# Kernel tuning notes

Hardware: AMD Instinct MI355X
Metric: run time of the kernel (lower is better)

Reference implementation:

```python
import jax, jax.numpy as jnp
import numpy as np

N_PARTICLES = 3_000_000
N_CVS = 30_000
N_MODELS = 8
FEATS = [64, 64, 64, 64]
E0, E1 = 2.0, 3.0
LN_EPS = 1e-5


def _dihedral(p):
    # p: [4,3] -> scalar dihedral angle (standard atan2 formulation)
    b1 = p[1] - p[0]
    b2 = p[2] - p[1]
    b3 = p[3] - p[2]
    n1 = jnp.cross(b1, b2)
    n2 = jnp.cross(b2, b3)
    m1 = jnp.cross(n1, b2 / jnp.linalg.norm(b2))
    return jnp.arctan2(jnp.dot(m1, n2), jnp.dot(n1, n2))


def _ensemble_energy(cvs, gamma, beta, Ws, bs):
    # cvs: [n_cvs] -> energy per model: [n_models]
    x = jnp.concatenate([jnp.cos(cvs), jnp.sin(cvs)])  # [2*n_cvs]
    mu = jnp.mean(x)
    var = jnp.mean((x - mu) ** 2)
    x = (x - mu) / jnp.sqrt(var + LN_EPS) * gamma + beta  # LayerNorm
    h = x[None, None, :]  # [1,1,2n] broadcasts against [M,2n,f]
    for i in range(len(Ws) - 1):
        h = jax.nn.relu(jnp.matmul(h, Ws[i]) + bs[i])  # [M,1,f]
    h = jnp.matmul(h, Ws[-1]) + bs[-1]  # [M,1,1]
    return h[:, 0, 0]  # [M]  (squeeze(-1) then batch dim 1)


def _uncertainty_weight(model_div):
    iswitch = (E1 - model_div) / (E1 - E0)
    fl = jnp.floor(iswitch)
    smooth = 0.5 * (1.0 + jnp.cos(jnp.pi * (1.0 - iswitch)))
    # heaviside(floor(iswitch), smooth): 1 if floor>0, smooth if floor==0, 0 if floor<0
    return jnp.where(fl > 0, 1.0, jnp.where(fl < 0, 0.0, smooth)).astype(model_div.dtype)


def setup_inputs() -> dict:
    key = jax.random.key(0)
    ks = jax.random.split(key, 16)
    positions = jax.random.normal(ks[0], (N_PARTICLES, 3), jnp.float32) * 3.0
    boxvectors = jnp.diag(jnp.full((3,), 10.0, dtype=jnp.float32))
    colvar_idx = jax.random.randint(ks[1], (N_CVS, 4), 0, N_PARTICLES)
    dims = [2 * N_CVS] + FEATS + [1]
    inp = {"positions": positions, "boxvectors": boxvectors, "colvar_idx": colvar_idx,
           "gamma": jnp.ones((2 * N_CVS,), jnp.float32),
           "beta": jnp.zeros((2 * N_CVS,), jnp.float32)}
    for i in range(5):
        bound = 1.0 / np.sqrt(dims[i])  # kaiming_uniform-like bound
        inp[f"W{i}"] = jax.random.uniform(ks[2 + i], (N_MODELS, dims[i], dims[i + 1]),
                                           jnp.float32, -bound, bound)
        inp[f"b{i}"] = jnp.zeros((N_MODELS, 1, dims[i + 1]), jnp.float32)
    return inp


def reference(positions, boxvectors, colvar_idx, gamma, beta,
              W0, b0, W1, b1, W2, b2, W3, b3, W4, b4):
    Ws = [W0, W1, W2, W3, W4]
    bs = [b0, b1, b2, b3, b4]
    boxsize = jnp.diag(boxvectors)  # [3]
    pos = positions - jnp.floor(positions / boxsize) * boxsize  # PBC wrap
    quads = pos[colvar_idx.reshape(-1)].reshape(-1, 4, 3)  # [n_cvs,4,3]
    cvs, dcvs_dx = jax.vmap(jax.value_and_grad(_dihedral))(quads)  # [n],[n,4,3]

    efn = lambda c: _ensemble_energy(c, gamma, beta, Ws, bs)  # [M]
    energy = efn(cvs)  # [M]
    mean_forces = -jax.jacrev(efn)(cvs)  # [M, n_cvs]: grad of -energy[m] wrt cvs

    model_div = jnp.sqrt(jnp.mean(jnp.var(mean_forces, axis=0, ddof=1)))
    sigma = _uncertainty_weight(model_div)
    mf = jnp.mean(mean_forces, axis=0)  # [n_cvs]
    contrib = (mf[:, None, None] * dcvs_dx).reshape(-1, 3)  # [n_cvs*4,3]
    forces = jnp.zeros_like(pos).at[colvar_idx.reshape(-1)].add(contrib)
    return energy.mean() * sigma, forces * sigma
```

## Files before the change

kernel.cpp:

```cpp
#include <hip/hip_runtime.h>
#include <math.h>

#define NCV   30000
#define NX    60000
#define NM    8
#define LN_EPSF 1e-5f
#define NFORCE 9000000

#define NB_CV 512
#define JB    96
#define SLAB  625
#define NBX   235
#define NB_MF 118

#define WS_XRAW   0
#define WS_DCV    60000
#define WS_G      420000
#define WS_LNP    900000
#define WS_Z0P    901024
#define WS_DZ0    950176
#define WS_E      950688
#define WS_SGP    950696
#define WS_SGXP   952576
#define WS_VARSUM 954456
#define WS_TICKET 954457
#define WS_SIGMA  954458
#define WS_FLAG   954459

struct F3 { float x, y, z; };
__device__ __forceinline__ F3 f3sub(F3 a, F3 b){ return {a.x-b.x, a.y-b.y, a.z-b.z}; }
__device__ __forceinline__ F3 f3add(F3 a, F3 b){ return {a.x+b.x, a.y+b.y, a.z+b.z}; }
__device__ __forceinline__ F3 f3scale(F3 a, float s){ return {a.x*s, a.y*s, a.z*s}; }
__device__ __forceinline__ float f3dot(F3 a, F3 b){ return a.x*b.x + a.y*b.y + a.z*b.z; }
__device__ __forceinline__ F3 f3cross(F3 a, F3 b){
  return { a.y*b.z - a.z*b.y, a.z*b.x - a.x*b.z, a.x*b.y - a.y*b.x };
}

__device__ __forceinline__ void compute_mu_inv(const float* __restrict__ ws, float* out2, int tid) {
  if (tid < 64) {
    float a = 0.f, b = 0.f;
    #pragma unroll 4
    for (int k = tid; k < NB_CV; k += 64) { a += ws[WS_LNP + k]; b += ws[WS_LNP + NB_CV + k]; }
    #pragma unroll
    for (int o = 1; o < 64; o <<= 1) { a += __shfl_xor(a, o); b += __shfl_xor(b, o); }
    if (tid == 0) {
      float mu  = a * (1.f / NX);
      float var = b * (1.f / NX) - mu * mu;
      out2[0] = mu;
      out2[1] = 1.f / sqrtf(var + LN_EPSF);
    }
  }
}

__global__ void k_cv(const float* __restrict__ pos, const float* __restrict__ box,
                     const int* __restrict__ idx, float* __restrict__ ws,
                     float* __restrict__ out) {
  int tid = threadIdx.x;
  int gtid = blockIdx.x * 256 + tid;

  {
    float4 z4 = {0.f, 0.f, 0.f, 0.f};
    float4* fz = (float4*)(out + 4);
    const int NF4 = (NFORCE - 4) / 4;
    for (int i = gtid; i < NF4; i += NB_CV * 256) fz[i] = z4;
    if (gtid == 0) {
      out[1] = 0.f; out[2] = 0.f; out[3] = 0.f; out[NFORCE] = 0.f;
      ws[WS_VARSUM] = 0.f;
      ((unsigned int*)ws)[WS_TICKET] = 0u;
      ((unsigned int*)ws)[WS_FLAG]   = 0u;
    }
  }

  float cx = 0.f, cx2 = 0.f;
  int i = gtid;
  if (i < NCV) {
    float bx = box[0], by = box[4], bz = box[8];
    int4 q4 = *(const int4*)(idx + i*4);
    int pidx[4] = {q4.x, q4.y, q4.z, q4.w};
    F3 p[4];
    #pragma unroll
    for (int a = 0; a < 4; a++) {
      int pi = pidx[a];
      float X = pos[(size_t)pi*3 + 0];
      float Y = pos[(size_t)pi*3 + 1];
      float Z = pos[(size_t)pi*3 + 2];
      X -= floorf(X / bx) * bx;
      Y -= floorf(Y / by) * by;
      Z -= floorf(Z / bz) * bz;
      p[a] = {X, Y, Z};
    }
    F3 b1 = f3sub(p[1], p[0]);
    F3 b2 = f3sub(p[2], p[1]);
    F3 b3 = f3sub(p[3], p[2]);
    F3 n1 = f3cross(b1, b2);
    F3 n2 = f3cross(b2, b3);
    float L = sqrtf(f3dot(b2, b2));
    F3 u = f3scale(b2, 1.f / L);
    F3 m1 = f3cross(n1, u);
    float yv = f3dot(m1, n2);
    float xv = f3dot(n1, n2);
    float h = sqrtf(xv*xv + yv*yv);
    float cphi = xv / h;
    float sphi = yv / h;

    float invd = 1.f / (h*h);
    float dX = -yv * invd;
    float dY =  xv * invd;
    F3 dn1 = f3scale(n2, dX);
    F3 dn2 = f3scale(n1, dX);
    F3 dm1 = f3scale(n2, dY);
    dn2 = f3add(dn2, f3scale(m1, dY));
    dn1 = f3add(dn1, f3cross(u, dm1));
    F3 du = f3cross(dm1, n1);
    float ud = f3dot(u, du);
    F3 db2 = f3scale(f3sub(du, f3scale(u, ud)), 1.f / L);
    db2 = f3add(db2, f3cross(b3, dn2));
    F3 db3 = f3cross(dn2, b2);
    F3 db1 = f3cross(b2, dn1);
    db2 = f3add(db2, f3cross(dn1, b1));

    F3 g0 = f3scale(db1, -1.f);
    F3 g1 = f3sub(db1, db2);
    F3 g2 = f3sub(db2, db3);
    F3 g3 = db3;

    ws[WS_XRAW + i]       = cphi;
    ws[WS_XRAW + NCV + i] = sphi;
    ws[WS_DCV + 0*NCV  + i] = g0.x; ws[WS_DCV + 1*NCV  + i] = g0.y; ws[WS_DCV + 2*NCV  + i] = g0.z;
    ws[WS_DCV + 3*NCV  + i] = g1.x; ws[WS_DCV + 4*NCV  + i] = g1.y; ws[WS_DCV + 5*NCV  + i] = g1.z;
    ws[WS_DCV + 6*NCV  + i] = g2.x; ws[WS_DCV + 7*NCV  + i] = g2.y; ws[WS_DCV + 8*NCV  + i] = g2.z;
    ws[WS_DCV + 9*NCV  + i] = g3.x; ws[WS_DCV + 10*NCV + i] = g3.y; ws[WS_DCV + 11*NCV + i] = g3.z;

    cx  = cphi + sphi;
    cx2 = cphi*cphi + sphi*sphi;
  }

  #pragma unroll
  for (int o = 1; o < 64; o <<= 1) { cx += __shfl_xor(cx, o); cx2 += __shfl_xor(cx2, o); }
  __shared__ float sa[4], sb[4];
  int w = tid >> 6, l = tid & 63;
  if (l == 0) { sa[w] = cx; sb[w] = cx2; }
  __syncthreads();
  if (tid == 0) {
    ws[WS_LNP + blockIdx.x]         = sa[0] + sa[1] + sa[2] + sa[3];
    ws[WS_LNP + NB_CV + blockIdx.x] = sb[0] + sb[1] + sb[2] + sb[3];
  }
}

__global__ __launch_bounds__(256, 2)
void k_z0(const float4* __restrict__ W0, const float* __restrict__ gamma,
          const float* __restrict__ beta, float* __restrict__ ws) {
  __shared__ float stats[2];
  __shared__ float yl[SLAB];
  __shared__ float red[4][16][4];
  int tid = threadIdx.x;
  int jb = blockIdx.x, m = blockIdx.y;
  int j0 = jb * SLAB;

  compute_mu_inv(ws, stats, tid);
  __syncthreads();
  float mu = stats[0], inv = stats[1];
  for (int jj = tid; jj < SLAB; jj += 256) {
    int gj = j0 + jj;
    yl[jj] = (ws[WS_XRAW + gj] - mu) * inv * gamma[gj] + beta[gj];
  }
  __syncthreads();

  int k4 = tid & 15;
  int r  = tid >> 4;
  const float4* Wm = W0 + (size_t)m * NX * 16;
  float4 acc = {0.f, 0.f, 0.f, 0.f};
  #pragma unroll 4
  for (int j = r; j < SLAB; j += 16) {
    float y = yl[j];
    float4 wv = Wm[(size_t)(j0 + j) * 16 + k4];
    acc.x += y * wv.x; acc.y += y * wv.y; acc.z += y * wv.z; acc.w += y * wv.w;
  }
  #pragma unroll
  for (int o = 16; o <= 32; o <<= 1) {
    acc.x += __shfl_xor(acc.x, o); acc.y += __shfl_xor(acc.y, o);
    acc.z += __shfl_xor(acc.z, o); acc.w += __shfl_xor(acc.w, o);
  }
  int w = tid >> 6, l = tid & 63;
  if (l < 16) {
    red[w][l][0] = acc.x; red[w][l][1] = acc.y; red[w][l][2] = acc.z; red[w][l][3] = acc.w;
  }
  __syncthreads();
  if (tid < 64) {
    int kk4 = tid & 15, c = tid >> 4;
    float v = red[0][kk4][c] + red[1][kk4][c] + red[2][kk4][c] + red[3][kk4][c];
    ws[WS_Z0P + ((size_t)m * JB + jb) * 64 + kk4 * 4 + c] = v;
  }
}

__global__ void k_mlp(const float* __restrict__ ws_ro, const float* __restrict__ b0,
                      const float* __restrict__ W1, const float* __restrict__ b1,
                      const float* __restrict__ W2, const float* __restrict__ b2,
                      const float* __restrict__ W3, const float* __restrict__ b3,
                      const float* __restrict__ W4, const float* __restrict__ b4,
                      float* __restrict__ ws) {
  int m = blockIdx.x;
  int tid = threadIdx.x;
  int k = tid & 63, q = tid >> 6;
  __shared__ float Wl[3][64*65];
  __shared__ float hs[4][64];
  __shared__ float part[256];
  __shared__ float ds[64];

  const float* Wsrc0 = W1 + m*4096;
  const float* Wsrc1 = W2 + m*4096;
  const float* Wsrc2 = W3 + m*4096;
  for (int e = tid; e < 4096; e += 256) {
    int t = e >> 6, kk = e & 63;
    Wl[0][t*65 + kk] = Wsrc0[e];
    Wl[1][t*65 + kk] = Wsrc1[e];
    Wl[2][t*65 + kk] = Wsrc2[e];
  }

  float p0 = 0.f;
  for (int jb = q; jb < JB; jb += 4)
    p0 += ws_ro[WS_Z0P + ((size_t)m * JB + jb) * 64 + k];
  part[tid] = p0;
  __syncthreads();
  if (tid < 64) {
    float a0 = b0[m*64 + k] + part[k] + part[64+k] + part[128+k] + part[192+k];
    hs[0][k] = fmaxf(a0, 0.f);
  }
  __syncthreads();

  #pragma unroll
  for (int l = 0; l < 3; l++) {
    float pp = 0.f;
    #pragma unroll
    for (int t0 = 0; t0 < 16; t0++) {
      int t = q*16 + t0;
      pp += hs[l][t] * Wl[l][t*65 + k];
    }
    part[tid] = pp;
    __syncthreads();
    if (tid < 64) {
      const float* bl = (l==0) ? b1 : (l==1) ? b2 : b3;
      float a = bl[m*64+k] + part[k] + part[64+k] + part[128+k] + part[192+k];
      hs[l+1][k] = fmaxf(a, 0.f);
    }
    __syncthreads();
  }

  if (tid < 64) {
    float w4k = W4[m*64 + k];
    float e = hs[3][k] * w4k;
    #pragma unroll
    for (int o = 1; o < 64; o <<= 1) e += __shfl_xor(e, o);
    if (k == 0) ws[WS_E + m] = e + b4[m];
    ds[k] = (hs[3][k] > 0.f) ? w4k : 0.f;
  }
  __syncthreads();

  #pragma unroll
  for (int l = 2; l >= 0; l--) {
    float pp = 0.f;
    int t = k;
    #pragma unroll
    for (int k0 = 0; k0 < 16; k0++) {
      int kk = q*16 + k0;
      pp += Wl[l][t*65 + kk] * ds[kk];
    }
    part[tid] = pp;
    __syncthreads();
    if (tid < 64) {
      float dh = part[k] + part[64+k] + part[128+k] + part[192+k];
      float dz = (hs[l][k] > 0.f) ? dh : 0.f;
      if (l == 0) ws[WS_DZ0 + m*64 + k] = dz;
      else        ds[k] = dz;
    }
    __syncthreads();
  }
}

__global__ __launch_bounds__(256, 2)
void k_bwdx(const float4* __restrict__ W0, const float* __restrict__ gamma,
            float* __restrict__ ws) {
  __shared__ float stats[2];
  __shared__ float dz[64];
  __shared__ float sa[4], sb[4];
  int tid = threadIdx.x;
  int m = blockIdx.y, blk = blockIdx.x;

  compute_mu_inv(ws, stats, tid);
  if (tid >= 64 && tid < 128) dz[tid - 64] = ws[WS_DZ0 + m*64 + (tid - 64)];
  __syncthreads();
  float mu = stats[0], inv = stats[1];

  int c = tid & 15;
  int g = tid >> 4;
  float4 d4 = ((const float4*)dz)[c];

  float sg = 0.f, sgx = 0.f;
  #pragma unroll
  for (int it = 0; it < 4; it++) {
    int jbase = blk * 256 + it * 64 + g;
    float4 wv[4];
    #pragma unroll
    for (int u = 0; u < 4; u++) {
      int j = jbase + u * 16;
      int jc = min(j, NX - 1);
      wv[u] = W0[((size_t)m * NX + jc) * 16 + c];
    }
    #pragma unroll
    for (int u = 0; u < 4; u++) {
      int j = jbase + u * 16;
      float dot = wv[u].x*d4.x + wv[u].y*d4.y + wv[u].z*d4.z + wv[u].w*d4.w;
      #pragma unroll
      for (int o = 1; o < 16; o <<= 1) dot += __shfl_xor(dot, o);
      if (c == 0 && j < NX) {
        float gg = dot * gamma[j];
        ws[WS_G + (size_t)m * NX + j] = gg;
        float xh = (ws[WS_XRAW + j] - mu) * inv;
        sg += gg; sgx += gg * xh;
      }
    }
  }
  #pragma unroll
  for (int o = 1; o < 64; o <<= 1) { sg += __shfl_xor(sg, o); sgx += __shfl_xor(sgx, o); }
  int w = tid >> 6, l = tid & 63;
  if (l == 0) { sa[w] = sg; sb[w] = sgx; }
  __syncthreads();
  if (tid == 0) {
    ws[WS_SGP  + m * NBX + blk] = sa[0] + sa[1] + sa[2] + sa[3];
    ws[WS_SGXP + m * NBX + blk] = sb[0] + sb[1] + sb[2] + sb[3];
  }
}

__global__ void k_mf(const int* __restrict__ idx, float* __restrict__ ws,
                     float* __restrict__ out) {
  __shared__ float stats[2];
  __shared__ float sSg[NM], sSgx[NM];
  __shared__ float sv[4];
  __shared__ float ssig;
  int tid = threadIdx.x;
  int w = tid >> 6, l = tid & 63;

  compute_mu_inv(ws, stats, tid);
  for (int m = w; m < NM; m += 4) {
    float a = 0.f, b = 0.f;
    #pragma unroll 2
    for (int bb = l; bb < NBX; bb += 64) { a += ws[WS_SGP + m*NBX + bb]; b += ws[WS_SGXP + m*NBX + bb]; }
    #pragma unroll
    for (int o = 1; o < 64; o <<= 1) { a += __shfl_xor(a, o); b += __shfl_xor(b, o); }
    if (l == 0) { sSg[m] = a * (1.f / NX); sSgx[m] = b * (1.f / NX); }
  }
  __syncthreads();
  float mu = stats[0], inv = stats[1];

  int i = blockIdx.x * 256 + tid;
  float v = 0.f, fm = 0.f;
  if (i < NCV) {
    float cph = ws[WS_XRAW + i], sph = ws[WS_XRAW + NCV + i];
    float xc = (cph - mu) * inv, xs = (sph - mu) * inv;
    float f[NM];
    #pragma unroll
    for (int m = 0; m < NM; m++) {
      float gc = ws[WS_G + (size_t)m * NX + i];
      float gs = ws[WS_G + (size_t)m * NX + NCV + i];
      float dxc = inv * (gc - sSg[m] - xc * sSgx[m]);
      float dxs = inv * (gs - sSg[m] - xs * sSgx[m]);
      float dE = dxc * (-sph) + dxs * cph;
      f[m] = -dE;
      fm += f[m];
    }
    fm *= (1.f / NM);
    float acc = 0.f;
    #pragma unroll
    for (int m = 0; m < NM; m++) { float d = f[m] - fm; acc += d * d; }
    v = acc * (1.f / (NM - 1));
  }
  #pragma unroll
  for (int o = 1; o < 64; o <<= 1) v += __shfl_xor(v, o);
  if (l == 0) sv[w] = v;
  __syncthreads();
  if (tid == 0) {
    atomicAdd(&ws[WS_VARSUM], sv[0] + sv[1] + sv[2] + sv[3]);
    __threadfence();
    unsigned int* tick = (unsigned int*)ws + WS_TICKET;
    unsigned int old = atomicAdd(tick, 1u);
    if (old == NB_MF - 1) {
      float tot = atomicAdd(&ws[WS_VARSUM], 0.0f);
      float md = sqrtf(tot * (1.f / NCV));
      float isw = (3.0f - md) / (3.0f - 2.0f);
      float fl = floorf(isw);
      float smooth = 0.5f * (1.f + cosf(3.14159265358979323846f * (1.f - isw)));
      float sigma = (fl > 0.f) ? 1.f : ((fl < 0.f) ? 0.f : smooth);
      float em = 0.f;
      #pragma unroll
      for (int m = 0; m < NM; m++) em += ws[WS_E + m];
      em *= (1.f / NM);
      out[0] = em * sigma;
      __hip_atomic_store(ws + WS_SIGMA, sigma, __ATOMIC_RELAXED, __HIP_MEMORY_SCOPE_AGENT);
      __hip_atomic_store((unsigned int*)ws + WS_FLAG, 1u, __ATOMIC_RELEASE, __HIP_MEMORY_SCOPE_AGENT);
    }
    while (__hip_atomic_load((unsigned int*)ws + WS_FLAG, __ATOMIC_ACQUIRE,
                             __HIP_MEMORY_SCOPE_AGENT) == 0u) {
      __builtin_amdgcn_s_sleep(8);
    }
    ssig = __hip_atomic_load(ws + WS_SIGMA, __ATOMIC_RELAXED, __HIP_MEMORY_SCOPE_AGENT);
  }
  __syncthreads();
  float sigma = ssig;

  if (i < NCV) {
    float d[12];
    #pragma unroll
    for (int r = 0; r < 12; r++) d[r] = ws[WS_DCV + r*NCV + i];
    int4 q4 = *(const int4*)(idx + i*4);
    float s = fm * sigma;
    float* fp = out + 1;
    atomicAdd(&fp[(size_t)q4.x*3 + 0], s*d[0]);
    atomicAdd(&fp[(size_t)q4.x*3 + 1], s*d[1]);
    atomicAdd(&fp[(size_t)q4.x*3 + 2], s*d[2]);
    atomicAdd(&fp[(size_t)q4.y*3 + 0], s*d[3]);
    atomicAdd(&fp[(size_t)q4.y*3 + 1], s*d[4]);
    atomicAdd(&fp[(size_t)q4.y*3 + 2], s*d[5]);
    atomicAdd(&fp[(size_t)q4.z*3 + 0], s*d[6]);
    atomicAdd(&fp[(size_t)q4.z*3 + 1], s*d[7]);
    atomicAdd(&fp[(size_t)q4.z*3 + 2], s*d[8]);
    atomicAdd(&fp[(size_t)q4.w*3 + 0], s*d[9]);
    atomicAdd(&fp[(size_t)q4.w*3 + 1], s*d[10]);
    atomicAdd(&fp[(size_t)q4.w*3 + 2], s*d[11]);
  }
}

extern "C" void kernel_launch(void* const* d_in, const int* in_sizes, int n_in,
                              void* d_out, int out_size, void* d_ws, size_t ws_size,
                              hipStream_t stream) {
  const float* pos   = (const float*)d_in[0];
  const float* box   = (const float*)d_in[1];
  const int*   idx   = (const int*)  d_in[2];
  const float* gamma = (const float*)d_in[3];
  const float* beta  = (const float*)d_in[4];
  const float* W0 = (const float*)d_in[5];
  const float* b0 = (const float*)d_in[6];
  const float* W1 = (const float*)d_in[7];
  const float* b1 = (const float*)d_in[8];
  const float* W2 = (const float*)d_in[9];
  const float* b2 = (const float*)d_in[10];
  const float* W3 = (const float*)d_in[11];
  const float* b3 = (const float*)d_in[12];
  const float* W4 = (const float*)d_in[13];
  const float* b4 = (const float*)d_in[14];
  float* ws  = (float*)d_ws;
  float* out = (float*)d_out;

  k_cv<<<NB_CV, 256, 0, stream>>>(pos, box, idx, ws, out);
  k_z0<<<dim3(JB, NM), 256, 0, stream>>>((const float4*)W0, gamma, beta, ws);
  k_mlp<<<NM, 256, 0, stream>>>(ws, b0, W1, b1, W2, b2, W3, b3, W4, b4, ws);
  k_bwdx<<<dim3(NBX, NM), 256, 0, stream>>>((const float4*)W0, gamma, ws);
  k_mf<<<NB_MF, 256, 0, stream>>>(idx, ws, out);
}
```

Baseline: 103.2 us.

## Fuse MLP into last z0 block via atomic ticket and enlarge slabs

Merges the small per-model MLP kernel into the W0 projection kernel. The last block to finish for each model, identified by an atomic ticket counter, runs the MLP forward and backward, which removes one kernel launch and its gap. The slab size grows from 625 to 1024 rows, so there are fewer blocks (59 per model) and fewer partials to reduce. The launch_bounds hints on k_z0 and k_bwdx are dropped. The trade-off is a larger shared-memory union and a serialized tail inside one block per model.

```diff
diff --git a/kernel.cpp b/kernel.cpp
--- a/kernel.cpp
+++ b/kernel.cpp
@@ -8,8 +8,7 @@
 #define NFORCE 9000000
 
 #define NB_CV 512
-#define JB    96
-#define SLAB  625
+#define JB    59
 #define NBX   235
 #define NB_MF 118
 
@@ -18,14 +17,15 @@
 #define WS_G      420000
 #define WS_LNP    900000
 #define WS_Z0P    901024
-#define WS_DZ0    950176
-#define WS_E      950688
-#define WS_SGP    950696
-#define WS_SGXP   952576
-#define WS_VARSUM 954456
-#define WS_TICKET 954457
-#define WS_SIGMA  954458
-#define WS_FLAG   954459
+#define WS_DZ0    931232
+#define WS_E      931744
+#define WS_SGP    931752
+#define WS_SGXP   933632
+#define WS_VARSUM 935512
+#define WS_TICKET 935513
+#define WS_SIGMA  935514
+#define WS_FLAG   935515
+#define WS_ZTICK  935516
 
 struct F3 { float x, y, z; };
 __device__ __forceinline__ F3 f3sub(F3 a, F3 b){ return {a.x-b.x, a.y-b.y, a.z-b.z}; }
@@ -68,6 +68,8 @@
       ws[WS_VARSUM] = 0.f;
       ((unsigned int*)ws)[WS_TICKET] = 0u;
       ((unsigned int*)ws)[WS_FLAG]   = 0u;
+      #pragma unroll
+      for (int m = 0; m < NM; m++) ((unsigned int*)ws)[WS_ZTICK + m] = 0u;
     }
   }
 
@@ -147,22 +149,29 @@
   }
 }
 
-__global__ __launch_bounds__(256, 2)
-void k_z0(const float4* __restrict__ W0, const float* __restrict__ gamma,
-          const float* __restrict__ beta, float* __restrict__ ws) {
-  __shared__ float stats[2];
-  __shared__ float yl[SLAB];
-  __shared__ float red[4][16][4];
+__global__ void k_z0(const float4* __restrict__ W0, const float* __restrict__ gamma,
+                     const float* __restrict__ beta,
+                     const float* __restrict__ b0,
+                     const float* __restrict__ W1, const float* __restrict__ b1,
+                     const float* __restrict__ W2, const float* __restrict__ b2,
+                     const float* __restrict__ W3, const float* __restrict__ b3,
+                     const float* __restrict__ W4, const float* __restrict__ b4,
+                     float* __restrict__ ws) {
+  __shared__ union {
+    struct { float stats[2]; float yl[1024]; float red[4][16][4]; float lastflag; } z;
+    struct { float Wl[3][64*65]; float hs[4][64]; float part[256]; float ds[64]; } mlp;
+  } sm;
   int tid = threadIdx.x;
   int jb = blockIdx.x, m = blockIdx.y;
-  int j0 = jb * SLAB;
-
-  compute_mu_inv(ws, stats, tid);
-  __syncthreads();
-  float mu = stats[0], inv = stats[1];
-  for (int jj = tid; jj < SLAB; jj += 256) {
+  int j0 = jb * 1024;
+  int jcount = min(1024, NX - j0);
+
+  compute_mu_inv(ws, sm.z.stats, tid);
+  __syncthreads();
+  float mu = sm.z.stats[0], inv = sm.z.stats[1];
+  for (int jj = tid; jj < 1024; jj += 256) {
     int gj = j0 + jj;
-    yl[jj] = (ws[WS_XRAW + gj] - mu) * inv * gamma[gj] + beta[gj];
+    sm.z.yl[jj] = (gj < NX) ? ((ws[WS_XRAW + gj] - mu) * inv * gamma[gj] + beta[gj]) : 0.f;
   }
   __syncthreads();
 
@@ -171,8 +180,8 @@
   const float4* Wm = W0 + (size_t)m * NX * 16;
   float4 acc = {0.f, 0.f, 0.f, 0.f};
   #pragma unroll 4
-  for (int j = r; j < SLAB; j += 16) {
-    float y = yl[j];
+  for (int j = r; j < jcount; j += 16) {
+    float y = sm.z.yl[j];
     float4 wv = Wm[(size_t)(j0 + j) * 16 + k4];
     acc.x += y * wv.x; acc.y += y * wv.y; acc.z += y * wv.z; acc.w += y * wv.w;
   }
@@ -183,103 +192,101 @@
   }
   int w = tid >> 6, l = tid & 63;
   if (l < 16) {
-    red[w][l][0] = acc.x; red[w][l][1] = acc.y; red[w][l][2] = acc.z; red[w][l][3] = acc.w;
+    sm.z.red[w][l][0] = acc.x; sm.z.red[w][l][1] = acc.y;
+    sm.z.red[w][l][2] = acc.z; sm.z.red[w][l][3] = acc.w;
   }
   __syncthreads();
   if (tid < 64) {
     int kk4 = tid & 15, c = tid >> 4;
-    float v = red[0][kk4][c] + red[1][kk4][c] + red[2][kk4][c] + red[3][kk4][c];
+    float v = sm.z.red[0][kk4][c] + sm.z.red[1][kk4][c] +
+              sm.z.red[2][kk4][c] + sm.z.red[3][kk4][c];
     ws[WS_Z0P + ((size_t)m * JB + jb) * 64 + kk4 * 4 + c] = v;
   }
-}
-
-__global__ void k_mlp(const float* __restrict__ ws_ro, const float* __restrict__ b0,
-                      const float* __restrict__ W1, const float* __restrict__ b1,
-                      const float* __restrict__ W2, const float* __restrict__ b2,
-                      const float* __restrict__ W3, const float* __restrict__ b3,
-                      const float* __restrict__ W4, const float* __restrict__ b4,
-                      float* __restrict__ ws) {
-  int m = blockIdx.x;
-  int tid = threadIdx.x;
-  int k = tid & 63, q = tid >> 6;
-  __shared__ float Wl[3][64*65];
-  __shared__ float hs[4][64];
-  __shared__ float part[256];
-  __shared__ float ds[64];
-
-  const float* Wsrc0 = W1 + m*4096;
-  const float* Wsrc1 = W2 + m*4096;
-  const float* Wsrc2 = W3 + m*4096;
-  for (int e = tid; e < 4096; e += 256) {
-    int t = e >> 6, kk = e & 63;
-    Wl[0][t*65 + kk] = Wsrc0[e];
-    Wl[1][t*65 + kk] = Wsrc1[e];
-    Wl[2][t*65 + kk] = Wsrc2[e];
-  }
-
-  float p0 = 0.f;
-  for (int jb = q; jb < JB; jb += 4)
-    p0 += ws_ro[WS_Z0P + ((size_t)m * JB + jb) * 64 + k];
-  part[tid] = p0;
-  __syncthreads();
-  if (tid < 64) {
-    float a0 = b0[m*64 + k] + part[k] + part[64+k] + part[128+k] + part[192+k];
-    hs[0][k] = fmaxf(a0, 0.f);
-  }
-  __syncthreads();
-
-  #pragma unroll
-  for (int l = 0; l < 3; l++) {
-    float pp = 0.f;
-    #pragma unroll
-    for (int t0 = 0; t0 < 16; t0++) {
-      int t = q*16 + t0;
-      pp += hs[l][t] * Wl[l][t*65 + k];
-    }
-    part[tid] = pp;
+  __syncthreads();
+
+  if (tid == 0) {
+    __threadfence();
+    unsigned old = atomicAdd((unsigned*)ws + WS_ZTICK + m, 1u);
+    sm.z.lastflag = (old == JB - 1) ? 1.f : 0.f;
+  }
+  __syncthreads();
+  bool last = (sm.z.lastflag != 0.f);
+  __syncthreads();
+  if (!last) return;
+  __threadfence();
+
+  {
+    int k = tid & 63, q = tid >> 6;
+    const float* Wsrc0 = W1 + m*4096;
+    const float* Wsrc1 = W2 + m*4096;
+    const float* Wsrc2 = W3 + m*4096;
+    for (int e = tid; e < 4096; e += 256) {
+      int t = e >> 6, kk = e & 63;
+      sm.mlp.Wl[0][t*65 + kk] = Wsrc0[e];
+      sm.mlp.Wl[1][t*65 + kk] = Wsrc1[e];
+      sm.mlp.Wl[2][t*65 + kk] = Wsrc2[e];
+    }
+    float p0 = 0.f;
+    for (int jb2 = q; jb2 < JB; jb2 += 4)
+      p0 += __hip_atomic_load(ws + WS_Z0P + ((size_t)m * JB + jb2) * 64 + k,
+                              __ATOMIC_RELAXED, __HIP_MEMORY_SCOPE_AGENT);
+    sm.mlp.part[tid] = p0;
     __syncthreads();
     if (tid < 64) {
-      const float* bl = (l==0) ? b1 : (l==1) ? b2 : b3;
-      float a = bl[m*64+k] + part[k] + part[64+k] + part[128+k] + part[192+k];
-      hs[l+1][k] = fmaxf(a, 0.f);
+      float a0 = b0[m*64 + k] + sm.mlp.part[k] + sm.mlp.part[64+k] + sm.mlp.part[128+k] + sm.mlp.part[192+k];
+      sm.mlp.hs[0][k] = fmaxf(a0, 0.f);
     }
     __syncthreads();
-  }
-
-  if (tid < 64) {
-    float w4k = W4[m*64 + k];
-    float e = hs[3][k] * w4k;
-    #pragma unroll
-    for (int o = 1; o < 64; o <<= 1) e += __shfl_xor(e, o);
-    if (k == 0) ws[WS_E + m] = e + b4[m];
-    ds[k] = (hs[3][k] > 0.f) ? w4k : 0.f;
-  }
-  __syncthreads();
-
-  #pragma unroll
-  for (int l = 2; l >= 0; l--) {
-    float pp = 0.f;
-    int t = k;
-    #pragma unroll
-    for (int k0 = 0; k0 < 16; k0++) {
-      int kk = q*16 + k0;
-      pp += Wl[l][t*65 + kk] * ds[kk];
-    }
-    part[tid] = pp;
+    #pragma unroll
+    for (int ll = 0; ll < 3; ll++) {
+      float pp = 0.f;
+      #pragma unroll
+      for (int t0 = 0; t0 < 16; t0++) {
+        int t = q*16 + t0;
+        pp += sm.mlp.hs[ll][t] * sm.mlp.Wl[ll][t*65 + k];
+      }
+      sm.mlp.part[tid] = pp;
+      __syncthreads();
+      if (tid < 64) {
+        const float* bl = (ll==0) ? b1 : (ll==1) ? b2 : b3;
+        float a = bl[m*64+k] + sm.mlp.part[k] + sm.mlp.part[64+k] + sm.mlp.part[128+k] + sm.mlp.part[192+k];
+        sm.mlp.hs[ll+1][k] = fmaxf(a, 0.f);
+      }
+      __syncthreads();
+    }
+    if (tid < 64) {
+      float w4k = W4[m*64 + k];
+      float e = sm.mlp.hs[3][k] * w4k;
+      #pragma unroll
+      for (int o = 1; o < 64; o <<= 1) e += __shfl_xor(e, o);
+      if (k == 0) ws[WS_E + m] = e + b4[m];
+      sm.mlp.ds[k] = (sm.mlp.hs[3][k] > 0.f) ? w4k : 0.f;
+    }
     __syncthreads();
-    if (tid < 64) {
-      float dh = part[k] + part[64+k] + part[128+k] + part[192+k];
-      float dz = (hs[l][k] > 0.f) ? dh : 0.f;
-      if (l == 0) ws[WS_DZ0 + m*64 + k] = dz;
-      else        ds[k] = dz;
-    }
-    __syncthreads();
-  }
-}
-
-__global__ __launch_bounds__(256, 2)
-void k_bwdx(const float4* __restrict__ W0, const float* __restrict__ gamma,
-            float* __restrict__ ws) {
+    #pragma unroll
+    for (int ll = 2; ll >= 0; ll--) {
+      float pp = 0.f;
+      int t = k;
+      #pragma unroll
+      for (int k0 = 0; k0 < 16; k0++) {
+        int kk = q*16 + k0;
+        pp += sm.mlp.Wl[ll][t*65 + kk] * sm.mlp.ds[kk];
+      }
+      sm.mlp.part[tid] = pp;
+      __syncthreads();
+      if (tid < 64) {
+        float dh = sm.mlp.part[k] + sm.mlp.part[64+k] + sm.mlp.part[128+k] + sm.mlp.part[192+k];
+        float dz = (sm.mlp.hs[ll][k] > 0.f) ? dh : 0.f;
+        if (ll == 0) ws[WS_DZ0 + m*64 + k] = dz;
+        else         sm.mlp.ds[k] = dz;
+      }
+      __syncthreads();
+    }
+  }
+}
+
+__global__ void k_bwdx(const float4* __restrict__ W0, const float* __restrict__ gamma,
+                       float* __restrict__ ws) {
   __shared__ float stats[2];
   __shared__ float dz[64];
   __shared__ float sa[4], sb[4];
@@ -451,8 +458,8 @@
   float* out = (float*)d_out;
 
   k_cv<<<NB_CV, 256, 0, stream>>>(pos, box, idx, ws, out);
-  k_z0<<<dim3(JB, NM), 256, 0, stream>>>((const float4*)W0, gamma, beta, ws);
-  k_mlp<<<NM, 256, 0, stream>>>(ws, b0, W1, b1, W2, b2, W3, b3, W4, b4, ws);
+  k_z0<<<dim3(JB, NM), 256, 0, stream>>>((const float4*)W0, gamma, beta,
+                                         b0, W1, b1, W2, b2, W3, b3, W4, b4, ws);
   k_bwdx<<<dim3(NBX, NM), 256, 0, stream>>>((const float4*)W0, gamma, ws);
   k_mf<<<NB_MF, 256, 0, stream>>>(idx, ws, out);
 }
```

Measured after the change: 115.9 us. 12.3% more time.
